# Optimization experiments

Hardware: AMD Instinct MI355X
Metric: run time of the kernel (lower is better)

Reference implementation:

```python
import jax, jax.numpy as jnp
import numpy as np

B, T, D = 512, 64, 512      # batch, encoder seq len, input_dim
H, A = 256, 256             # hidden_dim, attention_dim (= embed dim)
C = 96                      # num_classes = len(charsets) + 2
STEPS = 26                  # max_len_labels + 1
STD = 0.01


def setup_inputs() -> dict:
    key = jax.random.key(0)
    ks = jax.random.split(key, 14)
    n = lambda k, shape: STD * jax.random.normal(k, shape, jnp.float32)
    return {
        "img": jax.random.normal(ks[0], (B, T, D), jnp.float32),
        "label": jax.random.randint(ks[1], (B, STEPS), 0, C + 1),
        # MLP attention cell
        "Wx": n(ks[2], (A, D)), "bx": jnp.zeros((A,), jnp.float32),
        "Ws": n(ks[3], (A, H)), "bs": jnp.zeros((A,), jnp.float32),
        "Ww": n(ks[4], (1, A)), "bw": jnp.zeros((1,), jnp.float32),
        # target embedding (num_classes + 1 rows)
        "emb": n(ks[5], (C + 1, A)),
        # single-layer GRU, input size D + A, hidden H (torch gate order r,z,n)
        "Wih": n(ks[6], (3 * H, D + A)), "bih": jnp.zeros((3 * H,), jnp.float32),
        "Whh": n(ks[7], (3 * H, H)),     "bhh": jnp.zeros((3 * H,), jnp.float32),
        # output FC
        "Wfc": n(ks[8], (C, H)), "bfc": jnp.zeros((C,), jnp.float32),
    }


def reference(img, label, Wx, bx, Ws, bs, Ww, bw, emb, Wih, Whh, bih, bhh, Wfc, bfc):
    # Precompute xProj once: it is constant across decode steps.
    xProj = jnp.einsum('btd,ad->bta', img, Wx) + bx          # [B,T,A]
    # Teacher forcing: y at step 0 is 0 ([GO]); step i>=1 uses label[:, i].
    y_seq = label.at[:, 0].set(0)                            # [B,STEPS]

    def step(h, y):                                          # h: [B,H], y: [B]
        sProj = h @ Ws.T + bs                                # [B,A]
        e = jnp.tanh(sProj[:, None, :] + xProj)              # [B,T,A]
        v = jnp.einsum('bta,a->bt', e, Ww[0]) + bw[0]        # [B,T]
        alpha = jax.nn.softmax(v, axis=1)
        ctx = jnp.einsum('bt,btd->bd', alpha, img)           # [B,D]
        g = jnp.concatenate([emb[y], ctx], axis=1)           # [B,A+D]
        gi = g @ Wih.T + bih                                 # [B,3H]
        gh = h @ Whh.T + bhh                                 # [B,3H]
        r = jax.nn.sigmoid(gi[:, :H] + gh[:, :H])
        z = jax.nn.sigmoid(gi[:, H:2 * H] + gh[:, H:2 * H])
        nn_ = jnp.tanh(gi[:, 2 * H:] + r * gh[:, 2 * H:])
        h_new = (1.0 - z) * nn_ + z * h
        out = h_new @ Wfc.T + bfc                            # [B,C]
        return h_new, out

    h0 = jnp.zeros((img.shape[0], H), img.dtype)
    _, outs = jax.lax.scan(step, h0, y_seq.T)                # [STEPS,B,C]
    return jnp.transpose(outs, (1, 0, 2))                    # [B,STEPS,C]
```

## Files before the change

kernel.cpp:

```cpp
#include <hip/hip_runtime.h>
#include <math.h>

#define NB 512
#define NT 64
#define ND 512
#define NH 256
#define NA 256
#define NC 96
#define NSTEPS 26
#define NGRU 1152
#define KGRU 768

typedef __attribute__((ext_vector_type(8))) short short8;
typedef __attribute__((ext_vector_type(4))) float f32x4;

static __device__ __forceinline__ unsigned short f2bf(float f) {
    unsigned int u = __float_as_uint(f);
    unsigned int r = (u + 0x7FFFu + ((u >> 16) & 1u)) >> 16;
    return (unsigned short)r;
}
static __device__ __forceinline__ float bf2f(unsigned short u) {
    return __uint_as_float(((unsigned int)u) << 16);
}

__global__ __launch_bounds__(256) void k_prep(
    const float* __restrict__ Wx, const float* __restrict__ Ws,
    const float* __restrict__ Wfc, const float* __restrict__ Wih,
    const float* __restrict__ Whh,
    unsigned short* __restrict__ Wxbf, unsigned short* __restrict__ Wsbf,
    unsigned short* __restrict__ WfcT, unsigned short* __restrict__ Wp)
{
    const int idx = blockIdx.x * 256 + threadIdx.x;
    if (idx < NGRU * KGRU) {
        const int n = idx / KGRU, k = idx - n * KGRU;
        float val = 0.f;
        if (n < 1024) {
            const int j = n >> 2, g = n & 3;
            if (k < 512) {
                if (g == 0)      val = Wih[j * 768 + 256 + k];
                else if (g == 1) val = Wih[(256 + j) * 768 + 256 + k];
                else if (g == 2) val = Wih[(512 + j) * 768 + 256 + k];
            } else {
                const int kh = k - 512;
                if (g == 0)      val = Whh[j * 256 + kh];
                else if (g == 1) val = Whh[(256 + j) * 256 + kh];
                else if (g == 3) val = Whh[(512 + j) * 256 + kh];
            }
        } else if (n < 1120) {
            if (k >= 512) val = Wfc[(n - 1024) * 256 + (k - 512)];
        }
        Wp[idx] = f2bf(val);
    }
    if (idx < 131072) Wxbf[idx] = f2bf(Wx[idx]);
    if (idx < 65536)  Wsbf[idx] = f2bf(Ws[idx]);
    if (idx < 24576) {
        const int k = idx / 96, c = idx % 96;
        WfcT[idx] = f2bf(Wfc[c * 256 + k]);
    }
}

__global__ __launch_bounds__(256) void k_prep2(
    const float* __restrict__ emb, const float* __restrict__ Wih,
    const float* __restrict__ bih, const float* __restrict__ bhh,
    const float* __restrict__ bfc, float* __restrict__ P)
{
    const int y = blockIdx.x;
    const int n = blockIdx.y * 256 + threadIdx.x;
    __shared__ float embS[256];
    embS[threadIdx.x] = emb[y * 256 + threadIdx.x];
    __syncthreads();
    if (n >= NGRU) return;

    float bias = 0.f;
    const float* src = nullptr;
    if (n < 1024) {
        const int j = n >> 2, g = n & 3;
        if (g == 0)      { bias = bih[j] + bhh[j];             src = Wih + (size_t)j * 768; }
        else if (g == 1) { bias = bih[256 + j] + bhh[256 + j]; src = Wih + (size_t)(256 + j) * 768; }
        else if (g == 2) { bias = bih[512 + j];                src = Wih + (size_t)(512 + j) * 768; }
        else             { bias = bhh[512 + j]; }
    } else if (n < 1120) {
        bias = bfc[n - 1024];
    }
    float sp = bias;
    if (src) {
#pragma unroll 8
        for (int k = 0; k < 256; ++k) sp = fmaf(embS[k], src[k], sp);
    }
    P[(size_t)y * NGRU + n] = sp;
}

__global__ __launch_bounds__(256) void k_convert(
    const float* __restrict__ img, unsigned short* __restrict__ imgbf)
{
    const int idx = (blockIdx.x * 256 + threadIdx.x) * 8;
    const float4 v0 = *(const float4*)(img + idx);
    const float4 v1 = *(const float4*)(img + idx + 4);
    short8 o;
    o[0] = (short)f2bf(v0.x); o[1] = (short)f2bf(v0.y);
    o[2] = (short)f2bf(v0.z); o[3] = (short)f2bf(v0.w);
    o[4] = (short)f2bf(v1.x); o[5] = (short)f2bf(v1.y);
    o[6] = (short)f2bf(v1.z); o[7] = (short)f2bf(v1.w);
    *(short8*)(imgbf + idx) = o;
}

__global__ __launch_bounds__(256) void k_xproj(
    const float* __restrict__ img, const unsigned short* __restrict__ imgbf,
    int use_bf, const unsigned short* __restrict__ Wxbf,
    const float* __restrict__ bx, unsigned short* __restrict__ xProjbf)
{
    __shared__ unsigned short As[64][40];
    __shared__ unsigned short Bs[64][40];

    const int tid = threadIdx.x;
    const int lane = tid & 63;
    const int w = tid >> 6;
    const int l15 = lane & 15;
    const int q = lane >> 4;
    const int bm = blockIdx.x * 64;
    const int bn = blockIdx.y * 64;
    const int srow = tid >> 2;
    const int sc0 = (tid & 3) * 8;

    f32x4 acc[4];
#pragma unroll
    for (int i = 0; i < 4; ++i) acc[i] = (f32x4){0.f, 0.f, 0.f, 0.f};

    for (int k0 = 0; k0 < ND; k0 += 32) {
        if (use_bf) {
            *(short8*)&As[srow][sc0] =
                *(const short8*)(imgbf + (size_t)(bm + srow) * ND + k0 + sc0);
        } else {
            const float* ap = img + (size_t)(bm + srow) * ND + k0 + sc0;
            const float4 v0 = *(const float4*)ap;
            const float4 v1 = *(const float4*)(ap + 4);
            short8 av;
            av[0] = (short)f2bf(v0.x); av[1] = (short)f2bf(v0.y);
            av[2] = (short)f2bf(v0.z); av[3] = (short)f2bf(v0.w);
            av[4] = (short)f2bf(v1.x); av[5] = (short)f2bf(v1.y);
            av[6] = (short)f2bf(v1.z); av[7] = (short)f2bf(v1.w);
            *(short8*)&As[srow][sc0] = av;
        }
        *(short8*)&Bs[srow][sc0] =
            *(const short8*)(Wxbf + (size_t)(bn + srow) * ND + k0 + sc0);
        __syncthreads();

        const short8 bf = *(const short8*)&Bs[w * 16 + l15][q * 8];
#pragma unroll
        for (int mt = 0; mt < 4; ++mt) {
            const short8 af = *(const short8*)&As[mt * 16 + l15][q * 8];
            acc[mt] = __builtin_amdgcn_mfma_f32_16x16x32_bf16(af, bf, acc[mt], 0, 0, 0);
        }
        __syncthreads();
    }

#pragma unroll
    for (int mt = 0; mt < 4; ++mt) {
        const int col = bn + w * 16 + l15;
        const float bxv = bx[col];
#pragma unroll
        for (int r = 0; r < 4; ++r) {
            const int row = bm + mt * 16 + q * 4 + r;
            xProjbf[(size_t)row * NA + col] = f2bf(acc[mt][r] + bxv);
        }
    }
}

__global__ __launch_bounds__(128) void k_gru(
    const unsigned short* __restrict__ Ain, unsigned short* __restrict__ Aout,
    const unsigned short* __restrict__ Wp, const float* __restrict__ P,
    const int* __restrict__ label, float* __restrict__ h,
    float* __restrict__ out, int s)
{
    __shared__ unsigned short Af[16][776];
    __shared__ unsigned short Bs[64][72];
    __shared__ float CS[16][65];
    __shared__ int yS[16];

    const int tid = threadIdx.x;
    const int lane = tid & 63;
    const int w = tid >> 6;
    const int l15 = lane & 15;
    const int q = lane >> 4;
    const int bm = blockIdx.x * 16;
    const int bn = blockIdx.y * 64;

    if (tid < 16) yS[tid] = (s == 0) ? 0 : label[(bm + tid) * NSTEPS + s];

#pragma unroll
    for (int i = 0; i < 12; ++i) {
        const int c = tid + 128 * i;
        const int row = c / 96;
        const int col8 = (c - row * 96) * 8;
        *(short8*)&Af[row][col8] =
            *(const short8*)(Ain + (size_t)(bm + row) * KGRU + col8);
    }

    f32x4 acc[2];
    acc[0] = (f32x4){0.f, 0.f, 0.f, 0.f};
    acc[1] = (f32x4){0.f, 0.f, 0.f, 0.f};

    for (int k0 = 0; k0 < KGRU; k0 += 64) {
#pragma unroll
        for (int i = 0; i < 4; ++i) {
            const int c = tid + 128 * i;
            const int row = c >> 3, col8 = (c & 7) * 8;
            *(short8*)&Bs[row][col8] =
                *(const short8*)(Wp + (size_t)(bn + row) * KGRU + k0 + col8);
        }
        __syncthreads();
#pragma unroll
        for (int kk = 0; kk < 64; kk += 32) {
            const short8 af = *(const short8*)&Af[l15][k0 + kk + q * 8];
#pragma unroll
            for (int nt = 0; nt < 2; ++nt) {
                const short8 bf = *(const short8*)&Bs[(w * 2 + nt) * 16 + l15][kk + q * 8];
                acc[nt] = __builtin_amdgcn_mfma_f32_16x16x32_bf16(af, bf, acc[nt], 0, 0, 0);
            }
        }
        __syncthreads();
    }

    if (blockIdx.y < 16) {
#pragma unroll
        for (int nt = 0; nt < 2; ++nt) {
            const int cl = (w * 2 + nt) * 16 + l15;
            const float pv0 = P[(size_t)yS[q * 4 + 0] * NGRU + bn + cl];
            const float pv1 = P[(size_t)yS[q * 4 + 1] * NGRU + bn + cl];
            const float pv2 = P[(size_t)yS[q * 4 + 2] * NGRU + bn + cl];
            const float pv3 = P[(size_t)yS[q * 4 + 3] * NGRU + bn + cl];
            CS[q * 4 + 0][cl] = acc[nt][0] + pv0;
            CS[q * 4 + 1][cl] = acc[nt][1] + pv1;
            CS[q * 4 + 2][cl] = acc[nt][2] + pv2;
            CS[q * 4 + 3][cl] = acc[nt][3] + pv3;
        }
        __syncthreads();
#pragma unroll
        for (int it = 0; it < 2; ++it) {
            const int u = tid + 128 * it;
            const int row = u >> 4;
            const int jl = u & 15;
            const float r_pre = CS[row][4 * jl + 0];
            const float z_pre = CS[row][4 * jl + 1];
            const float ni    = CS[row][4 * jl + 2];
            const float nh    = CS[row][4 * jl + 3];
            const float r = 1.f / (1.f + expf(-r_pre));
            const float z = 1.f / (1.f + expf(-z_pre));
            const float n = tanhf(fmaf(r, nh, ni));
            const int b = bm + row;
            const int j = (bn >> 2) + jl;
            const float hp = h[b * NH + j];
            const float hn = (1.f - z) * n + z * hp;
            h[b * NH + j] = hn;
            Aout[(size_t)b * KGRU + 512 + j] = f2bf(hn);
        }
    } else {
        if (s >= 1) {
#pragma unroll
            for (int nt = 0; nt < 2; ++nt) {
                const int col = bn + (w * 2 + nt) * 16 + l15;
                const int c = col - 1024;
                if (c < NC) {
#pragma unroll
                    for (int r = 0; r < 4; ++r) {
                        const int row = q * 4 + r;
                        out[((size_t)(bm + row) * NSTEPS + (s - 1)) * NC + c] =
                            acc[nt][r] + P[(size_t)yS[row] * NGRU + col];
                    }
                }
            }
        }
    }
}

__global__ __launch_bounds__(256) void k_sproj(
    const unsigned short* __restrict__ Ahs, const unsigned short* __restrict__ Wsbf,
    const float* __restrict__ bs, float* __restrict__ sProj, int init)
{
    const int tid = threadIdx.x;
    const int b0 = blockIdx.x * 64;
    const int n0 = blockIdx.y * 64;

    if (init) {
        const int c = tid & 63, rg = tid >> 6;
        const float bv = bs[n0 + c];
#pragma unroll
        for (int i = 0; i < 16; ++i)
            sProj[(size_t)(b0 + rg * 16 + i) * NA + n0 + c] = bv;
        return;
    }

    __shared__ unsigned short As[64][72];
    __shared__ unsigned short Bs[64][72];

    const int lane = tid & 63;
    const int w = tid >> 6;
    const int l15 = lane & 15;
    const int q = lane >> 4;

    f32x4 acc[4];
#pragma unroll
    for (int i = 0; i < 4; ++i) acc[i] = (f32x4){0.f, 0.f, 0.f, 0.f};

    for (int k0 = 0; k0 < NH; k0 += 64) {
#pragma unroll
        for (int rep = 0; rep < 2; ++rep) {
            const int ch = tid + rep * 256;
            const int row = ch >> 3, col8 = (ch & 7) * 8;
            *(short8*)&As[row][col8] =
                *(const short8*)(Ahs + (size_t)(b0 + row) * KGRU + 512 + k0 + col8);
            *(short8*)&Bs[row][col8] =
                *(const short8*)(Wsbf + (size_t)(n0 + row) * NH + k0 + col8);
        }
        __syncthreads();
#pragma unroll
        for (int kk = 0; kk < 64; kk += 32) {
            const short8 bf = *(const short8*)&Bs[w * 16 + l15][kk + q * 8];
#pragma unroll
            for (int mt = 0; mt < 4; ++mt) {
                const short8 af = *(const short8*)&As[mt * 16 + l15][kk + q * 8];
                acc[mt] = __builtin_amdgcn_mfma_f32_16x16x32_bf16(af, bf, acc[mt], 0, 0, 0);
            }
        }
        __syncthreads();
    }

    const int col = n0 + w * 16 + l15;
    const float bv = bs[col];
#pragma unroll
    for (int mt = 0; mt < 4; ++mt)
#pragma unroll
        for (int r = 0; r < 4; ++r)
            sProj[(size_t)(b0 + mt * 16 + q * 4 + r) * NA + col] = acc[mt][r] + bv;
}

__global__ __launch_bounds__(512) void k_att(
    float* __restrict__ h, unsigned short* __restrict__ Aout,
    const float* __restrict__ sProj,
    const unsigned short* __restrict__ imgbf, const float* __restrict__ imgf,
    int use_bf, const unsigned short* __restrict__ xProjbf,
    const float* __restrict__ Ww, const float* __restrict__ bw, int step)
{
    const int b = blockIdx.x;
    const int tid = threadIdx.x;
    const int lane = tid & 63;
    const int w = tid >> 6;

    __shared__ float sS[NA];
    __shared__ float wwS[NA];
    __shared__ float vS[NT];
    __shared__ float alphaS[NT];
    __shared__ float ctxS[8][512];

    if (tid < 256) {
        sS[tid] = sProj[b * NA + tid];
        wwS[tid] = Ww[tid];
        if (step < 0) {
            h[b * NH + tid] = 0.f;
            Aout[(size_t)b * KGRU + 512 + tid] = 0;
        }
    }
    __syncthreads();

    const int a0 = (lane & 31) * 8;
    float ss[8], ww[8];
#pragma unroll
    for (int i = 0; i < 8; ++i) {
        ss[i] = sS[a0 + i];
        ww[i] = wwS[a0 + i];
    }
    const float bw0 = bw[0];
#pragma unroll 2
    for (int p = 0; p < 4; ++p) {
        const int t = w * 8 + p * 2 + (lane >> 5);
        const short8 x8 = *(const short8*)(xProjbf + ((size_t)(b * NT + t)) * NA + a0);
        float s = 0.f;
#pragma unroll
        for (int i = 0; i < 8; ++i)
            s += ww[i] * tanhf(ss[i] + bf2f((unsigned short)x8[i]));
#pragma unroll
        for (int off = 16; off > 0; off >>= 1) s += __shfl_xor(s, off);
        if ((lane & 31) == 0) vS[t] = s + bw0;
    }
    __syncthreads();

    if (w == 0) {
        float v = vS[lane];
        float m = v;
#pragma unroll
        for (int off = 32; off > 0; off >>= 1) m = fmaxf(m, __shfl_xor(m, off));
        float e = expf(v - m);
        float ssum = e;
#pragma unroll
        for (int off = 32; off > 0; off >>= 1) ssum += __shfl_xor(ssum, off);
        alphaS[lane] = e / ssum;
    }
    __syncthreads();

    const int d0 = lane * 8;
    float c[8];
#pragma unroll
    for (int i = 0; i < 8; ++i) c[i] = 0.f;

    if (use_bf) {
        const unsigned short* ib = imgbf + (size_t)b * NT * ND + d0;
#pragma unroll 2
        for (int i = 0; i < 8; ++i) {
            const int t = w + 8 * i;
            const float al = alphaS[t];
            const short8 v = *(const short8*)(ib + (size_t)t * ND);
#pragma unroll
            for (int k = 0; k < 8; ++k)
                c[k] = fmaf(al, bf2f((unsigned short)v[k]), c[k]);
        }
    } else {
        const float* ib = imgf + (size_t)b * NT * ND + d0;
#pragma unroll 2
        for (int i = 0; i < 8; ++i) {
            const int t = w + 8 * i;
            const float al = alphaS[t];
            const float4 v0 = *(const float4*)(ib + (size_t)t * ND);
            const float4 v1 = *(const float4*)(ib + (size_t)t * ND + 4);
            c[0] = fmaf(al, v0.x, c[0]); c[1] = fmaf(al, v0.y, c[1]);
            c[2] = fmaf(al, v0.z, c[2]); c[3] = fmaf(al, v0.w, c[3]);
            c[4] = fmaf(al, v1.x, c[4]); c[5] = fmaf(al, v1.y, c[5]);
            c[6] = fmaf(al, v1.z, c[6]); c[7] = fmaf(al, v1.w, c[7]);
        }
    }
    *(f32x4*)&ctxS[w][d0] = (f32x4){c[0], c[1], c[2], c[3]};
    *(f32x4*)&ctxS[w][d0 + 4] = (f32x4){c[4], c[5], c[6], c[7]};
    __syncthreads();

    float cx = ctxS[0][tid] + ctxS[1][tid] + ctxS[2][tid] + ctxS[3][tid]
             + ctxS[4][tid] + ctxS[5][tid] + ctxS[6][tid] + ctxS[7][tid];
    Aout[(size_t)b * KGRU + tid] = f2bf(cx);
}

__global__ __launch_bounds__(128) void k_fc(
    const float* __restrict__ h, const unsigned short* __restrict__ WfcT,
    const float* __restrict__ bfc, float* __restrict__ out)
{
    const int b = blockIdx.x;
    const int j = threadIdx.x;
    __shared__ float hS[NH];
    hS[j] = h[b * NH + j];
    hS[128 + j] = h[b * NH + 128 + j];
    __syncthreads();
    if (j < NC) {
        float acc = bfc[j];
#pragma unroll 8
        for (int k = 0; k < NH; ++k)
            acc = fmaf(hS[k], bf2f(WfcT[k * NC + j]), acc);
        out[((size_t)b * NSTEPS + (NSTEPS - 1)) * NC + j] = acc;
    }
}

extern "C" void kernel_launch(void* const* d_in, const int* in_sizes, int n_in,
                              void* d_out, int out_size, void* d_ws, size_t ws_size,
                              hipStream_t stream)
{
    const float* img   = (const float*)d_in[0];
    const int*   label = (const int*)d_in[1];
    const float* Wx    = (const float*)d_in[2];
    const float* bx    = (const float*)d_in[3];
    const float* Ws    = (const float*)d_in[4];
    const float* bs    = (const float*)d_in[5];
    const float* Ww    = (const float*)d_in[6];
    const float* bw    = (const float*)d_in[7];
    const float* emb   = (const float*)d_in[8];
    const float* Wih   = (const float*)d_in[9];
    const float* bih   = (const float*)d_in[10];
    const float* Whh   = (const float*)d_in[11];
    const float* bhh   = (const float*)d_in[12];
    const float* Wfc   = (const float*)d_in[13];
    const float* bfc   = (const float*)d_in[14];
    float* out = (float*)d_out;

    float* ws = (float*)d_ws;
    float* h     = ws;
    float* sProj = h + 131072;
    float* P     = sProj + 131072;
    unsigned short* xProjbf = (unsigned short*)(P + 111744);
    unsigned short* A0   = xProjbf + 8388608;
    unsigned short* A1   = A0 + 393216;
    unsigned short* Wp   = A1 + 393216;
    unsigned short* Wxbf = Wp + 884736;
    unsigned short* Wsbf = Wxbf + 131072;
    unsigned short* WfcT = Wsbf + 65536;
    unsigned short* imgbf = WfcT + 24576;

    const size_t need_bf = (size_t)((char*)(imgbf + 16777216) - (char*)d_ws);
    const int use_bf = (ws_size >= need_bf) ? 1 : 0;

    k_prep<<<dim3(3456), dim3(256), 0, stream>>>(
        Wx, Ws, Wfc, Wih, Whh, Wxbf, Wsbf, WfcT, Wp);

    k_prep2<<<dim3(97, 5), dim3(256), 0, stream>>>(
        emb, Wih, bih, bhh, bfc, P);

    if (use_bf)
        k_convert<<<dim3(8192), dim3(256), 0, stream>>>(img, imgbf);

    k_xproj<<<dim3((NB * NT) / 64, NA / 64), dim3(256), 0, stream>>>(
        img, imgbf, use_bf, Wxbf, bx, xProjbf);

    k_sproj<<<dim3(8, 4), dim3(256), 0, stream>>>(A0, Wsbf, bs, sProj, 1);
    k_att<<<dim3(NB), dim3(512), 0, stream>>>(
        h, A0, sProj, imgbf, img, use_bf, xProjbf, Ww, bw, -1);

    for (int s = 0; s < NSTEPS; ++s) {
        unsigned short* Ain  = (s & 1) ? A1 : A0;
        unsigned short* Aout = (s & 1) ? A0 : A1;

        k_gru<<<dim3(32, 18), dim3(128), 0, stream>>>(
            Ain, Aout, Wp, P, label, h, out, s);

        if (s < NSTEPS - 1) {
            k_sproj<<<dim3(8, 4), dim3(256), 0, stream>>>(Aout, Wsbf, bs, sProj, 0);
            k_att<<<dim3(NB), dim3(512), 0, stream>>>(
                h, Aout, sProj, imgbf, img, use_bf, xProjbf, Ww, bw, s);
        }
    }

    k_fc<<<dim3(NB), dim3(128), 0, stream>>>(h, WfcT, bfc, out);
}
```

Measured before the change: 836.6 us.

## Double-buffer GEMM tiles, MFMA embedding projection, and use fast exp/tanh

Replaces the scalar embedding-projection prep kernel with a bf16 MFMA GEMM that uses new prepacked embedding and weight buffers plus a bias vector. Adds register-staged double buffering of shared-memory tiles in the xProj and GRU GEMMs, and widens the xProj K step to 64. Switches tanh, sigmoid and softmax exp to __expf-based approximations in the GRU and attention kernels. This trades some numerical precision and extra shared memory for fewer stalls on global loads and cheaper transcendental math.

```diff
diff --git a/kernel.cpp b/kernel.cpp
--- a/kernel.cpp
+++ b/kernel.cpp
@@ -22,13 +22,24 @@
 static __device__ __forceinline__ float bf2f(unsigned short u) {
     return __uint_as_float(((unsigned int)u) << 16);
 }
+static __device__ __forceinline__ float ftanh(float x) {
+    const float e = __expf(2.0f * x);
+    return 1.0f - 2.0f / (e + 1.0f);
+}
+static __device__ __forceinline__ float fsigm(float x) {
+    return 1.0f / (1.0f + __expf(-x));
+}
 
 __global__ __launch_bounds__(256) void k_prep(
     const float* __restrict__ Wx, const float* __restrict__ Ws,
     const float* __restrict__ Wfc, const float* __restrict__ Wih,
-    const float* __restrict__ Whh,
+    const float* __restrict__ Whh, const float* __restrict__ emb,
+    const float* __restrict__ bih, const float* __restrict__ bhh,
+    const float* __restrict__ bfc,
     unsigned short* __restrict__ Wxbf, unsigned short* __restrict__ Wsbf,
-    unsigned short* __restrict__ WfcT, unsigned short* __restrict__ Wp)
+    unsigned short* __restrict__ WfcT, unsigned short* __restrict__ Wp,
+    unsigned short* __restrict__ embbf, unsigned short* __restrict__ WihE,
+    float* __restrict__ biasv)
 {
     const int idx = blockIdx.x * 256 + threadIdx.x;
     if (idx < NGRU * KGRU) {
@@ -51,43 +62,93 @@
         }
         Wp[idx] = f2bf(val);
     }
+    if (idx < 294912) {
+        const int n = idx >> 8, k = idx & 255;
+        float val = 0.f;
+        if (n < 1024) {
+            const int j = n >> 2, g = n & 3;
+            if (g == 0)      val = Wih[j * 768 + k];
+            else if (g == 1) val = Wih[(256 + j) * 768 + k];
+            else if (g == 2) val = Wih[(512 + j) * 768 + k];
+        }
+        WihE[idx] = f2bf(val);
+    }
     if (idx < 131072) Wxbf[idx] = f2bf(Wx[idx]);
     if (idx < 65536)  Wsbf[idx] = f2bf(Ws[idx]);
+    if (idx < 32768) {
+        const int y = idx >> 8;
+        embbf[idx] = (y < 97) ? f2bf(emb[idx]) : 0;
+    }
     if (idx < 24576) {
         const int k = idx / 96, c = idx % 96;
         WfcT[idx] = f2bf(Wfc[c * 256 + k]);
     }
-}
-
-__global__ __launch_bounds__(256) void k_prep2(
-    const float* __restrict__ emb, const float* __restrict__ Wih,
-    const float* __restrict__ bih, const float* __restrict__ bhh,
-    const float* __restrict__ bfc, float* __restrict__ P)
-{
-    const int y = blockIdx.x;
-    const int n = blockIdx.y * 256 + threadIdx.x;
-    __shared__ float embS[256];
-    embS[threadIdx.x] = emb[y * 256 + threadIdx.x];
-    __syncthreads();
-    if (n >= NGRU) return;
-
-    float bias = 0.f;
-    const float* src = nullptr;
-    if (n < 1024) {
-        const int j = n >> 2, g = n & 3;
-        if (g == 0)      { bias = bih[j] + bhh[j];             src = Wih + (size_t)j * 768; }
-        else if (g == 1) { bias = bih[256 + j] + bhh[256 + j]; src = Wih + (size_t)(256 + j) * 768; }
-        else if (g == 2) { bias = bih[512 + j];                src = Wih + (size_t)(512 + j) * 768; }
-        else             { bias = bhh[512 + j]; }
-    } else if (n < 1120) {
-        bias = bfc[n - 1024];
-    }
-    float sp = bias;
-    if (src) {
-#pragma unroll 8
-        for (int k = 0; k < 256; ++k) sp = fmaf(embS[k], src[k], sp);
-    }
-    P[(size_t)y * NGRU + n] = sp;
+    if (idx < NGRU) {
+        float v = 0.f;
+        if (idx < 1024) {
+            const int j = idx >> 2, g = idx & 3;
+            if (g == 0)      v = bih[j] + bhh[j];
+            else if (g == 1) v = bih[256 + j] + bhh[256 + j];
+            else if (g == 2) v = bih[512 + j];
+            else             v = bhh[512 + j];
+        } else if (idx < 1120) {
+            v = bfc[idx - 1024];
+        }
+        biasv[idx] = v;
+    }
+}
+
+__global__ __launch_bounds__(256) void k_pemb(
+    const unsigned short* __restrict__ embbf, const unsigned short* __restrict__ WihE,
+    const float* __restrict__ biasv, float* __restrict__ P)
+{
+    __shared__ unsigned short As[64][72];
+    __shared__ unsigned short Bs[64][72];
+
+    const int tid = threadIdx.x;
+    const int lane = tid & 63;
+    const int w = tid >> 6;
+    const int l15 = lane & 15;
+    const int q = lane >> 4;
+    const int b0 = blockIdx.x * 64;
+    const int n0 = blockIdx.y * 64;
+
+    f32x4 acc[4];
+#pragma unroll
+    for (int i = 0; i < 4; ++i) acc[i] = (f32x4){0.f, 0.f, 0.f, 0.f};
+
+    for (int k0 = 0; k0 < 256; k0 += 64) {
+#pragma unroll
+        for (int rep = 0; rep < 2; ++rep) {
+            const int ch = tid + rep * 256;
+            const int row = ch >> 3, col8 = (ch & 7) * 8;
+            *(short8*)&As[row][col8] =
+                *(const short8*)(embbf + (size_t)(b0 + row) * 256 + k0 + col8);
+            *(short8*)&Bs[row][col8] =
+                *(const short8*)(WihE + (size_t)(n0 + row) * 256 + k0 + col8);
+        }
+        __syncthreads();
+#pragma unroll
+        for (int kk = 0; kk < 64; kk += 32) {
+            const short8 bf = *(const short8*)&Bs[w * 16 + l15][kk + q * 8];
+#pragma unroll
+            for (int mt = 0; mt < 4; ++mt) {
+                const short8 af = *(const short8*)&As[mt * 16 + l15][kk + q * 8];
+                acc[mt] = __builtin_amdgcn_mfma_f32_16x16x32_bf16(af, bf, acc[mt], 0, 0, 0);
+            }
+        }
+        __syncthreads();
+    }
+
+    const int col = n0 + w * 16 + l15;
+    const float bv = biasv[col];
+#pragma unroll
+    for (int mt = 0; mt < 4; ++mt)
+#pragma unroll
+        for (int r = 0; r < 4; ++r) {
+            const int y = b0 + mt * 16 + q * 4 + r;
+            if (y < 97) P[(size_t)y * NGRU + col] = acc[mt][r] + bv;
+        }
 }
 
 __global__ __launch_bounds__(256) void k_convert(
@@ -109,8 +170,8 @@
     int use_bf, const unsigned short* __restrict__ Wxbf,
     const float* __restrict__ bx, unsigned short* __restrict__ xProjbf)
 {
-    __shared__ unsigned short As[64][40];
-    __shared__ unsigned short Bs[64][40];
+    __shared__ unsigned short As[2][64][72];
+    __shared__ unsigned short Bs[2][64][72];
 
     const int tid = threadIdx.x;
     const int lane = tid & 63;
@@ -119,37 +180,57 @@
     const int q = lane >> 4;
     const int bm = blockIdx.x * 64;
     const int bn = blockIdx.y * 64;
-    const int srow = tid >> 2;
-    const int sc0 = (tid & 3) * 8;
+    const int row0 = tid >> 3, col80 = (tid & 7) * 8;
+    const int row1 = (tid + 256) >> 3, col81 = col80;
 
     f32x4 acc[4];
 #pragma unroll
     for (int i = 0; i < 4; ++i) acc[i] = (f32x4){0.f, 0.f, 0.f, 0.f};
 
-    for (int k0 = 0; k0 < ND; k0 += 32) {
-        if (use_bf) {
-            *(short8*)&As[srow][sc0] =
-                *(const short8*)(imgbf + (size_t)(bm + srow) * ND + k0 + sc0);
-        } else {
-            const float* ap = img + (size_t)(bm + srow) * ND + k0 + sc0;
-            const float4 v0 = *(const float4*)ap;
-            const float4 v1 = *(const float4*)(ap + 4);
-            short8 av;
-            av[0] = (short)f2bf(v0.x); av[1] = (short)f2bf(v0.y);
-            av[2] = (short)f2bf(v0.z); av[3] = (short)f2bf(v0.w);
-            av[4] = (short)f2bf(v1.x); av[5] = (short)f2bf(v1.y);
-            av[6] = (short)f2bf(v1.z); av[7] = (short)f2bf(v1.w);
-            *(short8*)&As[srow][sc0] = av;
-        }
-        *(short8*)&Bs[srow][sc0] =
-            *(const short8*)(Wxbf + (size_t)(bn + srow) * ND + k0 + sc0);
-        __syncthreads();
-
-        const short8 bf = *(const short8*)&Bs[w * 16 + l15][q * 8];
-#pragma unroll
-        for (int mt = 0; mt < 4; ++mt) {
-            const short8 af = *(const short8*)&As[mt * 16 + l15][q * 8];
-            acc[mt] = __builtin_amdgcn_mfma_f32_16x16x32_bf16(af, bf, acc[mt], 0, 0, 0);
+    auto loadA = [&](int row, int col8, int k0) -> short8 {
+        if (use_bf)
+            return *(const short8*)(imgbf + (size_t)(bm + row) * ND + k0 + col8);
+        const float* ap = img + (size_t)(bm + row) * ND + k0 + col8;
+        const float4 v0 = *(const float4*)ap;
+        const float4 v1 = *(const float4*)(ap + 4);
+        short8 av;
+        av[0] = (short)f2bf(v0.x); av[1] = (short)f2bf(v0.y);
+        av[2] = (short)f2bf(v0.z); av[3] = (short)f2bf(v0.w);
+        av[4] = (short)f2bf(v1.x); av[5] = (short)f2bf(v1.y);
+        av[6] = (short)f2bf(v1.z); av[7] = (short)f2bf(v1.w);
+        return av;
+    };
+
+    *(short8*)&As[0][row0][col80] = loadA(row0, col80, 0);
+    *(short8*)&As[0][row1][col81] = loadA(row1, col81, 0);
+    *(short8*)&Bs[0][row0][col80] = *(const short8*)(Wxbf + (size_t)(bn + row0) * ND + col80);
+    *(short8*)&Bs[0][row1][col81] = *(const short8*)(Wxbf + (size_t)(bn + row1) * ND + col81);
+    __syncthreads();
+
+    for (int it = 0; it < 8; ++it) {
+        const int cur = it & 1;
+        short8 na0, na1, nb0, nb1;
+        if (it < 7) {
+            const int k0n = (it + 1) * 64;
+            na0 = loadA(row0, col80, k0n);
+            na1 = loadA(row1, col81, k0n);
+            nb0 = *(const short8*)(Wxbf + (size_t)(bn + row0) * ND + k0n + col80);
+            nb1 = *(const short8*)(Wxbf + (size_t)(bn + row1) * ND + k0n + col81);
+        }
+#pragma unroll
+        for (int kk = 0; kk < 64; kk += 32) {
+            const short8 bf = *(const short8*)&Bs[cur][w * 16 + l15][kk + q * 8];
+#pragma unroll
+            for (int mt = 0; mt < 4; ++mt) {
+                const short8 af = *(const short8*)&As[cur][mt * 16 + l15][kk + q * 8];
+                acc[mt] = __builtin_amdgcn_mfma_f32_16x16x32_bf16(af, bf, acc[mt], 0, 0, 0);
+            }
+        }
+        if (it < 7) {
+            *(short8*)&As[cur ^ 1][row0][col80] = na0;
+            *(short8*)&As[cur ^ 1][row1][col81] = na1;
+            *(short8*)&Bs[cur ^ 1][row0][col80] = nb0;
+            *(short8*)&Bs[cur ^ 1][row1][col81] = nb1;
         }
         __syncthreads();
     }
@@ -173,7 +254,7 @@
     float* __restrict__ out, int s)
 {
     __shared__ unsigned short Af[16][776];
-    __shared__ unsigned short Bs[64][72];
+    __shared__ unsigned short Bs[2][64][72];
     __shared__ float CS[16][65];
     __shared__ int yS[16];
 
@@ -195,27 +276,47 @@
         *(short8*)&Af[row][col8] =
             *(const short8*)(Ain + (size_t)(bm + row) * KGRU + col8);
     }
+#pragma unroll
+    for (int i = 0; i < 4; ++i) {
+        const int c = tid + 128 * i;
+        const int row = c >> 3, col8 = (c & 7) * 8;
+        *(short8*)&Bs[0][row][col8] =
+            *(const short8*)(Wp + (size_t)(bn + row) * KGRU + col8);
+    }
 
     f32x4 acc[2];
     acc[0] = (f32x4){0.f, 0.f, 0.f, 0.f};
     acc[1] = (f32x4){0.f, 0.f, 0.f, 0.f};
-
-    for (int k0 = 0; k0 < KGRU; k0 += 64) {
-#pragma unroll
-        for (int i = 0; i < 4; ++i) {
-            const int c = tid + 128 * i;
-            const int row = c >> 3, col8 = (c & 7) * 8;
-            *(short8*)&Bs[row][col8] =
-                *(const short8*)(Wp + (size_t)(bn + row) * KGRU + k0 + col8);
-        }
-        __syncthreads();
+    __syncthreads();
+
+    for (int it = 0; it < 12; ++it) {
+        const int cur = it & 1;
+        short8 nb[4];
+        if (it < 11) {
+            const int k0n = (it + 1) * 64;
+#pragma unroll
+            for (int i = 0; i < 4; ++i) {
+                const int c = tid + 128 * i;
+                const int row = c >> 3, col8 = (c & 7) * 8;
+                nb[i] = *(const short8*)(Wp + (size_t)(bn + row) * KGRU + k0n + col8);
+            }
+        }
+        const int k0 = it * 64;
 #pragma unroll
         for (int kk = 0; kk < 64; kk += 32) {
             const short8 af = *(const short8*)&Af[l15][k0 + kk + q * 8];
 #pragma unroll
             for (int nt = 0; nt < 2; ++nt) {
-                const short8 bf = *(const short8*)&Bs[(w * 2 + nt) * 16 + l15][kk + q * 8];
+                const short8 bf = *(const short8*)&Bs[cur][(w * 2 + nt) * 16 + l15][kk + q * 8];
                 acc[nt] = __builtin_amdgcn_mfma_f32_16x16x32_bf16(af, bf, acc[nt], 0, 0, 0);
+            }
+        }
+        if (it < 11) {
+#pragma unroll
+            for (int i = 0; i < 4; ++i) {
+                const int c = tid + 128 * i;
+                const int row = c >> 3, col8 = (c & 7) * 8;
+                *(short8*)&Bs[cur ^ 1][row][col8] = nb[i];
             }
         }
         __syncthreads();
@@ -225,14 +326,9 @@
 #pragma unroll
         for (int nt = 0; nt < 2; ++nt) {
             const int cl = (w * 2 + nt) * 16 + l15;
-            const float pv0 = P[(size_t)yS[q * 4 + 0] * NGRU + bn + cl];
-            const float pv1 = P[(size_t)yS[q * 4 + 1] * NGRU + bn + cl];
-            const float pv2 = P[(size_t)yS[q * 4 + 2] * NGRU + bn + cl];
-            const float pv3 = P[(size_t)yS[q * 4 + 3] * NGRU + bn + cl];
-            CS[q * 4 + 0][cl] = acc[nt][0] + pv0;
-            CS[q * 4 + 1][cl] = acc[nt][1] + pv1;
-            CS[q * 4 + 2][cl] = acc[nt][2] + pv2;
-            CS[q * 4 + 3][cl] = acc[nt][3] + pv3;
+#pragma unroll
+            for (int r = 0; r < 4; ++r)
+                CS[q * 4 + r][cl] = acc[nt][r] + P[(size_t)yS[q * 4 + r] * NGRU + bn + cl];
         }
         __syncthreads();
 #pragma unroll
@@ -244,9 +340,9 @@
             const float z_pre = CS[row][4 * jl + 1];
             const float ni    = CS[row][4 * jl + 2];
             const float nh    = CS[row][4 * jl + 3];
-            const float r = 1.f / (1.f + expf(-r_pre));
-            const float z = 1.f / (1.f + expf(-z_pre));
-            const float n = tanhf(fmaf(r, nh, ni));
+            const float r = fsigm(r_pre);
+            const float z = fsigm(z_pre);
+            const float n = ftanh(fmaf(r, nh, ni));
             const int b = bm + row;
             const int j = (bn >> 2) + jl;
             const float hp = h[b * NH + j];
@@ -377,7 +473,7 @@
         float s = 0.f;
 #pragma unroll
         for (int i = 0; i < 8; ++i)
-            s += ww[i] * tanhf(ss[i] + bf2f((unsigned short)x8[i]));
+            s += ww[i] * ftanh(ss[i] + bf2f((unsigned short)x8[i]));
 #pragma unroll
         for (int off = 16; off > 0; off >>= 1) s += __shfl_xor(s, off);
         if ((lane & 31) == 0) vS[t] = s + bw0;
@@ -389,7 +485,7 @@
         float m = v;
 #pragma unroll
         for (int off = 32; off > 0; off >>= 1) m = fmaxf(m, __shfl_xor(m, off));
-        float e = expf(v - m);
+        float e = __expf(v - m);
         float ssum = e;
 #pragma unroll
         for (int off = 32; off > 0; off >>= 1) ssum += __shfl_xor(ssum, off);
@@ -480,23 +576,26 @@
     float* h     = ws;
     float* sProj = h + 131072;
     float* P     = sProj + 131072;
-    unsigned short* xProjbf = (unsigned short*)(P + 111744);
-    unsigned short* A0   = xProjbf + 8388608;
-    unsigned short* A1   = A0 + 393216;
-    unsigned short* Wp   = A1 + 393216;
-    unsigned short* Wxbf = Wp + 884736;
-    unsigned short* Wsbf = Wxbf + 131072;
-    unsigned short* WfcT = Wsbf + 65536;
-    unsigned short* imgbf = WfcT + 24576;
+    float* biasv = P + 111744;
+    unsigned short* xProjbf = (unsigned short*)(biasv + 1280);
+    unsigned short* A0    = xProjbf + 8388608;
+    unsigned short* A1    = A0 + 393216;
+    unsigned short* Wp    = A1 + 393216;
+    unsigned short* Wxbf  = Wp + 884736;
+    unsigned short* Wsbf  = Wxbf + 131072;
+    unsigned short* WfcT  = Wsbf + 65536;
+    unsigned short* embbf = WfcT + 24576;
+    unsigned short* WihE  = embbf + 32768;
+    unsigned short* imgbf = WihE + 294912;
 
     const size_t need_bf = (size_t)((char*)(imgbf + 16777216) - (char*)d_ws);
     const int use_bf = (ws_size >= need_bf) ? 1 : 0;
 
     k_prep<<<dim3(3456), dim3(256), 0, stream>>>(
-        Wx, Ws, Wfc, Wih, Whh, Wxbf, Wsbf, WfcT, Wp);
-
-    k_prep2<<<dim3(97, 5), dim3(256), 0, stream>>>(
-        emb, Wih, bih, bhh, bfc, P);
+        Wx, Ws, Wfc, Wih, Whh, emb, bih, bhh, bfc,
+        Wxbf, Wsbf, WfcT, Wp, embbf, WihE, biasv);
+
+    k_pemb<<<dim3(2, 18), dim3(256), 0, stream>>>(embbf, WihE, biasv, P);
 
     if (use_bf)
         k_convert<<<dim3(8192), dim3(256), 0, stream>>>(img, imgbf);
```

Result: faster. 817.3 us (-2.3%).
